# Kernel optimization log

Hardware: AMD Instinct MI355X
Metric: run time of the kernel (lower is better)

## Reference

```python
import jax, jax.numpy as jnp
import numpy as np

BLOCK = 64       # _aether_cfg['block_size']
JL_DIM = 32      # epsilon_jl_bridge d_out
EPS_GOV = 0.5    # fixed governor eps (governor.target)
ROPE_BASE = 10000.0
RMS_EPS = 1e-6


def _normalize(x, axis=-1):
    n = jnp.sqrt(jnp.sum(x * x, axis=axis, keepdims=True))
    return x / jnp.maximum(n, 1e-12)


def _rms_norm(x):
    return x * jax.lax.rsqrt(jnp.mean(x * x, axis=-1, keepdims=True) + RMS_EPS)


def _rope(x, cos, sin):
    half = x.shape[-1] // 2
    x1, x2 = x[..., :half], x[..., half:]
    return jnp.concatenate([x1 * cos + x2 * sin, -x1 * sin + x2 * cos], axis=-1)


def setup_inputs() -> dict:
    key = jax.random.key(0)
    ks = jax.random.split(key, 6)
    B, S, Dm, H = 2, 2048, 2048, 16
    sc = 1.0 / np.sqrt(Dm)
    x = jax.random.normal(ks[0], (B, S, Dm), jnp.float32)
    Wq = jax.random.normal(ks[1], (Dm, Dm), jnp.float32) * sc
    Wk = jax.random.normal(ks[2], (Dm, Dm), jnp.float32) * sc
    Wv = jax.random.normal(ks[3], (Dm, Dm), jnp.float32) * sc
    Wo = jax.random.normal(ks[4], (Dm, Dm), jnp.float32) * sc
    q_gain = jnp.ones((H,), jnp.float32)
    return {"x": x, "Wq": Wq, "Wk": Wk, "Wv": Wv, "Wo": Wo, "q_gain": q_gain}


def reference(x, Wq, Wk, Wv, Wo, q_gain):
    B, S, Dm = x.shape
    H = q_gain.shape[0]
    Dh = Dm // H

    # QKV projections (bias-free linear, torch weight layout [out,in])
    q = (x @ Wq.T).reshape(B, S, H, Dh).transpose(0, 2, 1, 3)  # (B,H,S,Dh)
    k = (x @ Wk.T).reshape(B, S, H, Dh).transpose(0, 2, 1, 3)
    v = (x @ Wv.T).reshape(B, S, H, Dh).transpose(0, 2, 1, 3)

    # RoPE tables
    inv_freq = 1.0 / (ROPE_BASE ** (jnp.arange(0, Dh, 2, dtype=jnp.float32) / Dh))
    freqs = jnp.outer(jnp.arange(S, dtype=jnp.float32), inv_freq)  # (S,Dh/2)
    cos = jnp.cos(freqs)[None, None]
    sin = jnp.sin(freqs)[None, None]

    q = _rope(_rms_norm(q), cos, sin) * q_gain[None, :, None, None]
    k = _rope(_rms_norm(k), cos, sin)

    # --- aether sparse SDPA: JL block bounds -> top-k blocks -> gather -> SDPA ---
    N = S // BLOCK  # number of KV blocks (static)
    proj = jax.random.normal(jax.random.key(42), (Dh, JL_DIM), jnp.float32) / np.sqrt(JL_DIM)

    q_proj = _normalize(q.mean(axis=2, keepdims=True) @ proj)          # (B,H,1,JL)
    k_blocks = k.reshape(B, H, N, BLOCK, Dh)
    k_proj = _normalize(k_blocks @ proj)                               # (B,H,N,BLOCK,JL)
    centroids = _normalize(k_proj.mean(axis=3))                        # (B,H,N,JL)
    radii = jnp.clip(
        1.0 - jnp.min(jnp.sum(k_proj * centroids[:, :, :, None, :], axis=-1), axis=-1),
        0.0, 1.0)                                                      # (B,H,N)
    ub = jnp.einsum('bhqj,bhnj->bhqn', q_proj, centroids) + radii[:, :, None, :]
    scores = ub[:, :, 0, :]                                            # (B,H,N)
    # force-include the last two blocks (union in the original code)
    scores = scores.at[:, :, N - 2:].set(jnp.inf)

    n_keep = max(2, int(N * min(1.0, EPS_GOV))) + 2                    # static
    _, top_idx = jax.lax.top_k(scores, n_keep)                         # (B,H,n_keep)
    top_idx = jnp.sort(top_idx, axis=-1)
    idx = (top_idx[..., None] * BLOCK + jnp.arange(BLOCK)).reshape(B, H, -1)  # (B,H,K)

    k_s = jnp.take_along_axis(k, idx[..., None], axis=2)               # (B,H,K,Dh)
    v_s = jnp.take_along_axis(v, idx[..., None], axis=2)

    att = jax.nn.softmax(
        jnp.einsum('bhqd,bhkd->bhqk', q, k_s) / np.sqrt(Dh), axis=-1)  # (B,H,S,K)
    y = jnp.einsum('bhqk,bhkd->bhqd', att, v_s)                        # (B,H,S,Dh)

    y = y.transpose(0, 2, 1, 3).reshape(B, S, Dm)
    return y @ Wo.T
```

## Files before the change

kernel.cpp:

```cpp
#include <hip/hip_runtime.h>
#include <hip/hip_bf16.h>

#define B_ 2
#define S_ 2048
#define DM 2048
#define H_ 16
#define DH 128
#define NBLK 32
#define NKEEP 18
#define BH (B_ * H_)

typedef __attribute__((ext_vector_type(8))) short short8;
typedef __attribute__((ext_vector_type(8))) _Float16 f16x8;
typedef __attribute__((ext_vector_type(4))) _Float16 f16x4;
typedef __attribute__((ext_vector_type(4))) float f32x4;

#define GLOAD16(gp, lp)                                                        \
  __builtin_amdgcn_global_load_lds(                                            \
      (const __attribute__((address_space(1))) unsigned int*)(const void*)(gp),\
      (__attribute__((address_space(3))) unsigned int*)(void*)(lp), 16, 0, 0)

__device__ __forceinline__ unsigned short f32_to_bf16(float f) {
  unsigned u = __float_as_uint(f);
  unsigned r = (u + 0x7fffu + ((u >> 16) & 1u)) >> 16;
  return (unsigned short)r;
}
__device__ __forceinline__ float bf16_to_f32(unsigned short h) {
  return __uint_as_float(((unsigned)h) << 16);
}

__device__ __forceinline__ unsigned rotl32(unsigned x, int r) {
  return (x << r) | (x >> (32 - r));
}

__device__ __forceinline__ float erfinv_f32(float x) {
  float w = -log1pf(-x * x);
  float p;
  if (w < 5.0f) {
    w -= 2.5f;
    p = 2.81022636e-08f;
    p = fmaf(p, w, 3.43273939e-07f);
    p = fmaf(p, w, -3.5233877e-06f);
    p = fmaf(p, w, -4.39150654e-06f);
    p = fmaf(p, w, 0.00021858087f);
    p = fmaf(p, w, -0.00125372503f);
    p = fmaf(p, w, -0.00417768164f);
    p = fmaf(p, w, 0.246640727f);
    p = fmaf(p, w, 1.50140941f);
  } else {
    w = sqrtf(w) - 3.0f;
    p = -0.000200214257f;
    p = fmaf(p, w, 0.000100950558f);
    p = fmaf(p, w, 0.00134934322f);
    p = fmaf(p, w, -0.00367342844f);
    p = fmaf(p, w, 0.00573950773f);
    p = fmaf(p, w, -0.0076224613f);
    p = fmaf(p, w, 0.00943887047f);
    p = fmaf(p, w, 1.00167406f);
    p = fmaf(p, w, 2.83297682f);
  }
  return p * x;
}

__device__ __forceinline__ float bits_to_normal(unsigned b) {
  float f = __uint_as_float((b >> 9) | 0x3f800000u) - 1.0f;
  const float lo = -0.9999999403953552f;
  float u = fmaxf(lo, fmaf(f, 2.0f, lo));
  return 1.4142135623730951f * erfinv_f32(u);
}

__global__ void proj_kernel(float* __restrict__ proj) {
  int i = blockIdx.x * blockDim.x + threadIdx.x;
  if (i >= 4096) return;
  unsigned k0 = 0u, k1 = 42u;
  unsigned k2 = 0x1BD11BDAu ^ k0 ^ k1;
  unsigned x0 = 0u, x1 = (unsigned)i;
  x0 += k0; x1 += k1;
#define QR(r) { x0 += x1; x1 = rotl32(x1, r); x1 ^= x0; }
  QR(13) QR(15) QR(26) QR(6)   x0 += k1; x1 += k2 + 1u;
  QR(17) QR(29) QR(16) QR(24)  x0 += k2; x1 += k0 + 2u;
  QR(13) QR(15) QR(26) QR(6)   x0 += k0; x1 += k1 + 3u;
  QR(17) QR(29) QR(16) QR(24)  x0 += k1; x1 += k2 + 4u;
  QR(13) QR(15) QR(26) QR(6)   x0 += k2; x1 += k0 + 5u;
#undef QR
  proj[i] = bits_to_normal(x0 ^ x1) / 5.656854249492381f;
}

__global__ void rope_table_kernel(float* __restrict__ cosb, float* __restrict__ sinb) {
  int s = blockIdx.x;
  int j = threadIdx.x;
  double e = (double)(2 * j) / 128.0;
  double invf = 1.0 / pow(10000.0, e);
  float freq = (float)s * (float)invf;
  cosb[s * 64 + j] = (float)cos((double)freq);
  sinb[s * 64 + j] = (float)sin((double)freq);
}

__global__ __launch_bounds__(256) void split_x3_kernel(const float* __restrict__ in,
                                                       unsigned short* __restrict__ hi,
                                                       unsigned short* __restrict__ lo,
                                                       _Float16* __restrict__ f16,
                                                       int n4) {
  int i = blockIdx.x * blockDim.x + threadIdx.x;
  if (i >= n4) return;
  float4 v = ((const float4*)in)[i];
  ushort4 hv, lv;
  f16x4 fv;
  hv.x = f32_to_bf16(v.x); lv.x = f32_to_bf16(v.x - bf16_to_f32(hv.x)); fv[0] = (_Float16)v.x;
  hv.y = f32_to_bf16(v.y); lv.y = f32_to_bf16(v.y - bf16_to_f32(hv.y)); fv[1] = (_Float16)v.y;
  hv.z = f32_to_bf16(v.z); lv.z = f32_to_bf16(v.z - bf16_to_f32(hv.z)); fv[2] = (_Float16)v.z;
  hv.w = f32_to_bf16(v.w); lv.w = f32_to_bf16(v.w - bf16_to_f32(hv.w)); fv[3] = (_Float16)v.w;
  ((ushort4*)hi)[i] = hv;
  ((ushort4*)lo)[i] = lv;
  ((f16x4*)f16)[i] = fv;
}

__global__ __launch_bounds__(256) void split_kernel(const float* __restrict__ in,
                                                    unsigned short* __restrict__ hi,
                                                    unsigned short* __restrict__ lo,
                                                    int n4) {
  int i = blockIdx.x * blockDim.x + threadIdx.x;
  if (i >= n4) return;
  float4 v = ((const float4*)in)[i];
  ushort4 hv, lv;
  hv.x = f32_to_bf16(v.x); lv.x = f32_to_bf16(v.x - bf16_to_f32(hv.x));
  hv.y = f32_to_bf16(v.y); lv.y = f32_to_bf16(v.y - bf16_to_f32(hv.y));
  hv.z = f32_to_bf16(v.z); lv.z = f32_to_bf16(v.z - bf16_to_f32(hv.z));
  hv.w = f32_to_bf16(v.w); lv.w = f32_to_bf16(v.w - bf16_to_f32(hv.w));
  ((ushort4*)hi)[i] = hv;
  ((ushort4*)lo)[i] = lv;
}

__global__ __launch_bounds__(256) void split_f16_kernel(const float* __restrict__ in,
                                                        _Float16* __restrict__ f16,
                                                        int n4) {
  int i = blockIdx.x * blockDim.x + threadIdx.x;
  if (i >= n4) return;
  float4 v = ((const float4*)in)[i];
  f16x4 fv;
  fv[0] = (_Float16)v.x; fv[1] = (_Float16)v.y;
  fv[2] = (_Float16)v.z; fv[3] = (_Float16)v.w;
  ((f16x4*)f16)[i] = fv;
}

__global__ __launch_bounds__(512, 2) void mfma_gemm_k_sk(const unsigned short* __restrict__ Ahi,
                                                         const unsigned short* __restrict__ Alo,
                                                         const unsigned short* __restrict__ Whi,
                                                         const unsigned short* __restrict__ Wlo,
                                                         float* __restrict__ kp0,
                                                         float* __restrict__ kp1) {
  __shared__ char smem[131072];
  const int t = threadIdx.x, l = t & 63, w = t >> 6;
  const int lin = blockIdx.z * 128 + blockIdx.y * 8 + blockIdx.x;
  const int swz = (lin & 7) * 32 + (lin >> 3);
  const int kz = swz >> 7;
  const int idx = swz & 127;
  const int n0 = (idx & 7) * 256;
  const int m0 = (idx >> 3) * 256;
  const int kbase = kz * 1024;
  float* C = kz ? kp1 : kp0;
  const int wm = w >> 2, wn = w & 3;
  const int lr = l & 15;
  const int lg8 = (l >> 4) * 8;
  const size_t rstep = (size_t)16 * DM;

  const unsigned short* gAh = Ahi + (size_t)(m0 + w * 32 + lr) * DM + lg8;
  const unsigned short* gAl = Alo + (size_t)(m0 + w * 32 + lr) * DM + lg8;
  const unsigned short* gBh = Whi + (size_t)(n0 + w * 32 + lr) * DM + lg8;
  const unsigned short* gBl = Wlo + (size_t)(n0 + w * 32 + lr) * DM + lg8;

  f32x4 acc[8][4];
#pragma unroll
  for (int i = 0; i < 8; ++i)
#pragma unroll
    for (int j = 0; j < 4; ++j) acc[i][j] = (f32x4){0.f, 0.f, 0.f, 0.f};

  {
    char* base = smem + w * 2048;
    GLOAD16(gAh + kbase, base);
    GLOAD16(gAh + rstep + kbase, base + 1024);
    GLOAD16(gAl + kbase, base + 16384);
    GLOAD16(gAl + rstep + kbase, base + 16384 + 1024);
    GLOAD16(gBh + kbase, base + 32768);
    GLOAD16(gBh + rstep + kbase, base + 32768 + 1024);
    GLOAD16(gBl + kbase, base + 49152);
    GLOAD16(gBl + rstep + kbase, base + 49152 + 1024);
  }
  int cur = 0;

#define KQUAD(q)                                                                        \
  {                                                                                     \
    short8 ah0 = *(const short8*)(buf + (wm * 8 + 2 * (q)) * 1024 + l * 16);            \
    short8 ah1 = *(const short8*)(buf + (wm * 8 + 2 * (q) + 1) * 1024 + l * 16);        \
    short8 al0 = *(const short8*)(buf + 16384 + (wm * 8 + 2 * (q)) * 1024 + l * 16);    \
    short8 al1 = *(const short8*)(buf + 16384 + (wm * 8 + 2 * (q) + 1) * 1024 + l * 16);\
    __builtin_amdgcn_s_setprio(1);                                                      \
    _Pragma("unroll")                                                                   \
    for (int n = 0; n < 4; ++n) {                                                       \
      acc[2 * (q)][n] = __builtin_amdgcn_mfma_f32_16x16x32_bf16(ah0, bh[n], acc[2 * (q)][n], 0, 0, 0); \
      acc[2 * (q)][n] = __builtin_amdgcn_mfma_f32_16x16x32_bf16(ah0, bl[n], acc[2 * (q)][n], 0, 0, 0); \
      acc[2 * (q)][n] = __builtin_amdgcn_mfma_f32_16x16x32_bf16(al0, bh[n], acc[2 * (q)][n], 0, 0, 0); \
    }                                                                                   \
    _Pragma("unroll")                                                                   \
    for (int n = 0; n < 4; ++n) {                                                       \
      acc[2 * (q) + 1][n] = __builtin_amdgcn_mfma_f32_16x16x32_bf16(ah1, bh[n], acc[2 * (q) + 1][n], 0, 0, 0); \
      acc[2 * (q) + 1][n] = __builtin_amdgcn_mfma_f32_16x16x32_bf16(ah1, bl[n], acc[2 * (q) + 1][n], 0, 0, 0); \
      acc[2 * (q) + 1][n] = __builtin_amdgcn_mfma_f32_16x16x32_bf16(al1, bh[n], acc[2 * (q) + 1][n], 0, 0, 0); \
    }                                                                                   \
    __builtin_amdgcn_s_setprio(0);                                                      \
  }

  for (int k0 = kbase; k0 < kbase + 1024; k0 += 32) {
    const bool more = (k0 + 32 < kbase + 1024);
    char* buf = smem + cur * 65536;
    char* nb = smem + (cur ^ 1) * 65536 + w * 2048;
    const int kn = k0 + 32;

    if (more) {
      GLOAD16(gBh + kn, nb + 32768);
      GLOAD16(gBh + rstep + kn, nb + 32768 + 1024);
      asm volatile("s_waitcnt vmcnt(2)" ::: "memory");
    } else {
      asm volatile("s_waitcnt vmcnt(0)" ::: "memory");
    }
    __builtin_amdgcn_s_barrier();

    short8 bh[4], bl[4];
#pragma unroll
    for (int f = 0; f < 4; ++f) {
      bh[f] = *(const short8*)(buf + 32768 + (wn * 4 + f) * 1024 + l * 16);
      bl[f] = *(const short8*)(buf + 49152 + (wn * 4 + f) * 1024 + l * 16);
    }
    KQUAD(0);
    __builtin_amdgcn_s_barrier();

    if (more) {
      GLOAD16(gBl + kn, nb + 49152);
      GLOAD16(gBl + rstep + kn, nb + 49152 + 1024);
    }
    KQUAD(1);
    __builtin_amdgcn_s_barrier();

    if (more) {
      GLOAD16(gAh + kn, nb);
      GLOAD16(gAh + rstep + kn, nb + 1024);
    }
    KQUAD(2);
    __builtin_amdgcn_s_barrier();

    if (more) {
      GLOAD16(gAl + kn, nb + 16384);
      GLOAD16(gAl + rstep + kn, nb + 16384 + 1024);
    }
    KQUAD(3);
    __builtin_amdgcn_s_barrier();

    cur ^= 1;
  }
#undef KQUAD

#pragma unroll
  for (int m = 0; m < 8; ++m) {
    int row0 = m0 + wm * 128 + m * 16 + (l >> 4) * 4;
#pragma unroll
    for (int n = 0; n < 4; ++n) {
      int col = n0 + wn * 64 + n * 16 + (l & 15);
      int h = col >> 7, d = col & 127;
#pragma unroll
      for (int r = 0; r < 4; ++r) {
        int mm = row0 + r;
        int b = mm >> 11, s = mm & (S_ - 1);
        C[(((size_t)(b * H_ + h) * S_) + s) * DH + d] = acc[m][n][r];
      }
    }
  }
}

__global__ __launch_bounds__(512, 2) void mfma_gemm_qv(const _Float16* __restrict__ A,
                                                       const _Float16* __restrict__ W,
                                                       float* __restrict__ Cq,
                                                       _Float16* __restrict__ vt) {
  __shared__ char smem[65536];
  const int t = threadIdx.x, l = t & 63, w = t >> 6;
  const int lin = blockIdx.y * gridDim.x + blockIdx.x;
  const int swz = (lin & 7) * 32 + (lin >> 3);
  const int n0 = (swz & 15) * 256;
  const int m0 = (swz >> 4) * 256;
  const int wm = w >> 2, wn = w & 3;
  const int lr = l & 15;
  const int lg8 = (l >> 4) * 8;
  const size_t rstep = (size_t)16 * DM;

  const _Float16* gA = A + (size_t)(m0 + w * 32 + lr) * DM + lg8;
  const _Float16* gB = W + (size_t)(n0 + w * 32 + lr) * DM + lg8;

  f32x4 acc[8][4];
#pragma unroll
  for (int i = 0; i < 8; ++i)
#pragma unroll
    for (int j = 0; j < 4; ++j) acc[i][j] = (f32x4){0.f, 0.f, 0.f, 0.f};

  {
    char* base = smem + w * 2048;
    GLOAD16(gA, base);
    GLOAD16(gA + rstep, base + 1024);
    GLOAD16(gB, base + 16384);
    GLOAD16(gB + rstep, base + 16384 + 1024);
  }
  int cur = 0;

  for (int k0 = 0; k0 < DM; k0 += 32) {
    const bool more = (k0 + 32 < DM);
    char* buf = smem + cur * 32768;
    char* nb = smem + (cur ^ 1) * 32768 + w * 2048;
    const int kn = k0 + 32;

    if (more) {
      GLOAD16(gA + kn, nb);
      GLOAD16(gA + rstep + kn, nb + 1024);
      asm volatile("s_waitcnt vmcnt(2)" ::: "memory");
    } else {
      asm volatile("s_waitcnt vmcnt(0)" ::: "memory");
    }
    __builtin_amdgcn_s_barrier();

    f16x8 b[4];
#pragma unroll
    for (int j = 0; j < 4; ++j)
      b[j] = *(const f16x8*)(buf + 16384 + (wn * 4 + j) * 1024 + l * 16);
    __builtin_amdgcn_s_setprio(1);
#pragma unroll
    for (int i = 0; i < 4; ++i) {
      f16x8 a = *(const f16x8*)(buf + (wm * 8 + i) * 1024 + l * 16);
#pragma unroll
      for (int j = 0; j < 4; ++j)
        acc[i][j] = __builtin_amdgcn_mfma_f32_16x16x32_f16(a, b[j], acc[i][j], 0, 0, 0);
    }
    __builtin_amdgcn_s_setprio(0);
    __builtin_amdgcn_s_barrier();

    if (more) {
      GLOAD16(gB + kn, nb + 16384);
      GLOAD16(gB + rstep + kn, nb + 16384 + 1024);
    }
    __builtin_amdgcn_s_setprio(1);
#pragma unroll
    for (int i = 4; i < 8; ++i) {
      f16x8 a = *(const f16x8*)(buf + (wm * 8 + i) * 1024 + l * 16);
#pragma unroll
      for (int j = 0; j < 4; ++j)
        acc[i][j] = __builtin_amdgcn_mfma_f32_16x16x32_f16(a, b[j], acc[i][j], 0, 0, 0);
    }
    __builtin_amdgcn_s_setprio(0);
    __builtin_amdgcn_s_barrier();

    cur ^= 1;
  }

#pragma unroll
  for (int m = 0; m < 8; ++m) {
    int row0 = m0 + wm * 128 + m * 16 + (l >> 4) * 4;
#pragma unroll
    for (int n = 0; n < 4; ++n) {
      int col = n0 + wn * 64 + n * 16 + (l & 15);
      if (col < DM) {
        int h = col >> 7, d = col & 127;
#pragma unroll
        for (int r = 0; r < 4; ++r) {
          int mm = row0 + r;
          int b2 = mm >> 11, s = mm & (S_ - 1);
          Cq[(((size_t)(b2 * H_ + h) * S_) + s) * DH + d] = acc[m][n][r];
        }
      } else {
        int vcol = col - DM;
        int h = vcol >> 7, d = vcol & 127;
        int b2 = row0 >> 11, s0 = row0 & (S_ - 1);
        f16x4 vv;
        vv[0] = (_Float16)acc[m][n][0];
        vv[1] = (_Float16)acc[m][n][1];
        vv[2] = (_Float16)acc[m][n][2];
        vv[3] = (_Float16)acc[m][n][3];
        *(f16x4*)(vt + (((size_t)(b2 * H_ + h)) * DH + d) * S_ + s0) = vv;
      }
    }
  }
}

template <int MODE>
__global__ __launch_bounds__(256) void mfma_gemm_f16(const _Float16* __restrict__ A,
                                                     const _Float16* __restrict__ W,
                                                     void* __restrict__ Cout) {
  __shared__ char smem[65536];
  const int t = threadIdx.x, l = t & 63, w = t >> 6;
  const int lin = blockIdx.y * gridDim.x + blockIdx.x;
  const int cpx = (gridDim.x * gridDim.y) >> 3;
  const int swz = (lin & 7) * cpx + (lin >> 3);
  const int n0 = (swz % gridDim.x) * 128;
  const int m0 = (swz / gridDim.x) * 128;
  const int wm = w >> 1, wn = w & 1;
  const int lr = l & 15;
  const int lg8 = (l >> 4) * 8;

  auto STAGE = [&](int k0, int c) {
    char* base = smem + c * 32768;
#pragma unroll
    for (int f0 = 0; f0 < 4; ++f0) {
      int f = w * 4 + f0;
      int rb = f >> 1, kh = f & 1;
      GLOAD16(A + (size_t)(m0 + rb * 16 + lr) * DM + k0 + kh * 32 + lg8,
              base + f * 1024);
      GLOAD16(W + (size_t)(n0 + rb * 16 + lr) * DM + k0 + kh * 32 + lg8,
              base + 16384 + f * 1024);
    }
  };

  f32x4 acc[4][4];
#pragma unroll
  for (int i = 0; i < 4; ++i)
#pragma unroll
    for (int j = 0; j < 4; ++j) acc[i][j] = (f32x4){0.f, 0.f, 0.f, 0.f};

  STAGE(0, 0);
  int cur = 0;

  for (int k0 = 0; k0 < DM; k0 += 64) {
    if (k0 + 64 < DM) {
      STAGE(k0 + 64, cur ^ 1);
      asm volatile("s_waitcnt vmcnt(8)" ::: "memory");
    } else {
      asm volatile("s_waitcnt vmcnt(0)" ::: "memory");
    }
    __builtin_amdgcn_s_barrier();

    char* buf = smem + cur * 32768;
    f16x8 a[4][2], b[4][2];
#pragma unroll
    for (int i = 0; i < 4; ++i)
#pragma unroll
      for (int kh = 0; kh < 2; ++kh) {
        a[i][kh] = *(const f16x8*)(buf + ((wm * 4 + i) * 2 + kh) * 1024 + l * 16);
        b[i][kh] = *(const f16x8*)(buf + 16384 + ((wn * 4 + i) * 2 + kh) * 1024 + l * 16);
      }
    __builtin_amdgcn_s_setprio(1);
#pragma unroll
    for (int i = 0; i < 4; ++i)
#pragma unroll
      for (int j = 0; j < 4; ++j) {
        acc[i][j] = __builtin_amdgcn_mfma_f32_16x16x32_f16(a[i][0], b[j][0], acc[i][j], 0, 0, 0);
        acc[i][j] = __builtin_amdgcn_mfma_f32_16x16x32_f16(a[i][1], b[j][1], acc[i][j], 0, 0, 0);
      }
    __builtin_amdgcn_s_setprio(0);
    __builtin_amdgcn_s_barrier();
    cur ^= 1;
  }

#pragma unroll
  for (int i = 0; i < 4; ++i) {
    int row0 = m0 + wm * 64 + i * 16 + (l >> 4) * 4;
#pragma unroll
    for (int j = 0; j < 4; ++j) {
      int col = n0 + wn * 64 + j * 16 + (l & 15);
      if constexpr (MODE == 1) {
        float* C = (float*)Cout;
#pragma unroll
        for (int r = 0; r < 4; ++r)
          C[(size_t)(row0 + r) * DM + col] = acc[i][j][r];
      }
    }
  }
}

__global__ __launch_bounds__(256) void rmsrope_k_kernel(float* __restrict__ k,
                                                        const float* __restrict__ kp1,
                                                        _Float16* __restrict__ kf,
                                                        const float* __restrict__ cosb,
                                                        const float* __restrict__ sinb) {
  int w = threadIdx.x >> 6;
  int lane = threadIdx.x & 63;
  long r = (long)blockIdx.x * 4 + w;
  float* p = k + r * DH;
  const float* p1 = kp1 + r * DH;
  int s = (int)(r & (S_ - 1));
  float x1 = p[lane] + p1[lane];
  float x2 = p[lane + 64] + p1[lane + 64];
  float ss = fmaf(x1, x1, x2 * x2);
#pragma unroll
  for (int off = 32; off; off >>= 1) ss += __shfl_xor(ss, off);
  float rms = rsqrtf(ss * (1.0f / 128.0f) + 1e-6f);
  float n1 = x1 * rms, n2 = x2 * rms;
  float c = cosb[s * 64 + lane], sn = sinb[s * 64 + lane];
  float o1 = fmaf(n1, c, n2 * sn);
  float o2 = fmaf(-n1, sn, n2 * c);
  p[lane] = o1;
  p[lane + 64] = o2;
  kf[r * DH + lane] = (_Float16)o1;
  kf[r * DH + lane + 64] = (_Float16)o2;
}

__global__ __launch_bounds__(256) void rmsrope_q_kernel(float* __restrict__ q,
                                                        const float* __restrict__ cosb,
                                                        const float* __restrict__ sinb,
                                                        const float* __restrict__ qg) {
  int w = threadIdx.x >> 6;
  int lane = threadIdx.x & 63;
  long r = (long)blockIdx.x * 4 + w;
  float* p = q + r * DH;
  int s = (int)(r & (S_ - 1));
  int h = (int)((r >> 11) & (H_ - 1));
  float x1 = p[lane], x2 = p[lane + 64];
  float ss = fmaf(x1, x1, x2 * x2);
#pragma unroll
  for (int off = 32; off; off >>= 1) ss += __shfl_xor(ss, off);
  float rms = rsqrtf(ss * (1.0f / 128.0f) + 1e-6f);
  float n1 = x1 * rms, n2 = x2 * rms;
  float c = cosb[s * 64 + lane], sn = sinb[s * 64 + lane];
  float g = qg[h];
  float o1 = fmaf(n1, c, n2 * sn) * g;
  float o2 = fmaf(-n1, sn, n2 * c) * g;
  p[lane] = o1;
  p[lane + 64] = o2;
}

__global__ __launch_bounds__(256) void qmean_part_kernel(const float* __restrict__ q,
                                                         float* __restrict__ partial) {
  __shared__ float red[256];
  const int bh = blockIdx.x >> 4, chunk = blockIdx.x & 15;
  const int t = threadIdx.x;
  const int d = t & 127, half = t >> 7;
  const float* qb = q + ((size_t)bh * S_ + chunk * 128 + half * 64) * DH;
  float sum = 0.0f;
#pragma unroll 4
  for (int s = 0; s < 64; ++s) sum += qb[(size_t)s * DH + d];
  red[t] = sum;
  __syncthreads();
  if (t < 128) partial[(size_t)blockIdx.x * 128 + t] = red[t] + red[t + 128];
}

__global__ void qproj_kernel(const float* __restrict__ partial,
                             const float* __restrict__ proj,
                             float* __restrict__ qp) {
  __shared__ float meanq[128];
  __shared__ float qps[32];
  __shared__ float nrm;
  const int bh = blockIdx.x, t = threadIdx.x;
  float s = 0.0f;
#pragma unroll
  for (int c = 0; c < 16; ++c) s += partial[((size_t)bh * 16 + c) * 128 + t];
  meanq[t] = s * (1.0f / 2048.0f);
  __syncthreads();
  if (t < 32) {
    float sum = 0.0f;
    for (int d = 0; d < 128; ++d) sum = fmaf(meanq[d], proj[d * 32 + t], sum);
    qps[t] = sum;
  }
  __syncthreads();
  if (t == 0) {
    float sum = 0.0f;
    for (int j = 0; j < 32; ++j) sum += qps[j] * qps[j];
    nrm = 1.0f / fmaxf(sqrtf(sum), 1e-12f);
  }
  __syncthreads();
  if (t < 32) qp[bh * 32 + t] = qps[t] * nrm;
}

__global__ __launch_bounds__(256) void kscore_kernel(const float* __restrict__ k,
                                                     const float* __restrict__ proj,
                                                     const float* __restrict__ qp,
                                                     float* __restrict__ scores) {
  __shared__ float ps[128][32];
  __shared__ float kp[64][33];
  __shared__ float cent[33];
  __shared__ float nrm;
  const int bh = blockIdx.x >> 5, n = blockIdx.x & 31;
  const int t = threadIdx.x;
  for (int i = t; i < 4096; i += 256) ps[i >> 5][i & 31] = proj[i];
  const float* kn = k + ((size_t)bh * S_ + n * 64) * DH;
  __syncthreads();
  {
    int row = t >> 2, j0 = (t & 3) * 8;
    float accv[8];
#pragma unroll
    for (int jj = 0; jj < 8; ++jj) accv[jj] = 0.0f;
#pragma unroll 4
    for (int d = 0; d < 128; ++d) {
      float kv = kn[(size_t)row * DH + d];
#pragma unroll
      for (int jj = 0; jj < 8; ++jj) accv[jj] = fmaf(kv, ps[d][j0 + jj], accv[jj]);
    }
#pragma unroll
    for (int jj = 0; jj < 8; ++jj) kp[row][j0 + jj] = accv[jj];
  }
  __syncthreads();
  if (t < 64) {
    float sum = 0.0f;
    for (int j = 0; j < 32; ++j) sum += kp[t][j] * kp[t][j];
    float scl = 1.0f / fmaxf(sqrtf(sum), 1e-12f);
    for (int j = 0; j < 32; ++j) kp[t][j] *= scl;
  }
  __syncthreads();
  if (t < 32) {
    float sum = 0.0f;
    for (int r2 = 0; r2 < 64; ++r2) sum += kp[r2][t];
    cent[t] = sum * (1.0f / 64.0f);
  }
  __syncthreads();
  if (t == 0) {
    float sum = 0.0f;
    for (int j = 0; j < 32; ++j) sum += cent[j] * cent[j];
    nrm = 1.0f / fmaxf(sqrtf(sum), 1e-12f);
  }
  __syncthreads();
  if (t < 32) cent[t] *= nrm;
  __syncthreads();
  if (t < 64) {
    float dt = 0.0f;
    for (int j = 0; j < 32; ++j) dt = fmaf(kp[t][j], cent[j], dt);
#pragma unroll
    for (int off = 32; off; off >>= 1) dt = fminf(dt, __shfl_xor(dt, off));
    if (t == 0) {
      float radius = fminf(fmaxf(1.0f - dt, 0.0f), 1.0f);
      float dq = 0.0f;
      for (int j = 0; j < 32; ++j) dq = fmaf(qp[bh * 32 + j], cent[j], dq);
      scores[bh * 32 + n] = dq + radius;
    }
  }
}

__global__ void topk_kernel(const float* __restrict__ scores, int* __restrict__ top_idx) {
  if (threadIdx.x != 0) return;
  const int bh = blockIdx.x;
  float sc[NBLK];
  for (int j = 0; j < NBLK; ++j) sc[j] = scores[bh * 32 + j];
  sc[NBLK - 2] = INFINITY;
  sc[NBLK - 1] = INFINITY;
  int chosen[NKEEP];
  bool used[NBLK];
  for (int j = 0; j < NBLK; ++j) used[j] = false;
  for (int kk = 0; kk < NKEEP; ++kk) {
    int best = -1;
    float bv = 0.0f;
    for (int j = 0; j < NBLK; ++j)
      if (!used[j] && (best < 0 || sc[j] > bv)) { bv = sc[j]; best = j; }
    used[best] = true;
    chosen[kk] = best;
  }
  for (int a = 1; a < NKEEP; ++a) {
    int v2 = chosen[a], b2 = a - 1;
    while (b2 >= 0 && chosen[b2] > v2) { chosen[b2 + 1] = chosen[b2]; --b2; }
    chosen[b2 + 1] = v2;
  }
  for (int a = 0; a < NKEEP; ++a) top_idx[bh * NKEEP + a] = chosen[a];
}

__global__ __launch_bounds__(256) void attn_mfma_kernel(const float* __restrict__ q,
                                                        const _Float16* __restrict__ kf,
                                                        const _Float16* __restrict__ vt,
                                                        const int* __restrict__ top_idx,
                                                        _Float16* __restrict__ yf) {
  __shared__ char lds[74752];
  const int bh = blockIdx.x >> 5;
  const int qt = blockIdx.x & 31;
  const int t = threadIdx.x, l = t & 63, w = t >> 6;
  const int lr = l & 15, lg = l >> 4;
  const float scale = 0.08838834764831843f;

  f16x8 qf[4];
  {
    const float* qbase = q + ((size_t)(bh * S_ + qt * 64 + w * 16 + lr)) * DH + lg * 8;
#pragma unroll
    for (int dc = 0; dc < 4; ++dc) {
      float4 v0 = *(const float4*)(qbase + dc * 32);
      float4 v1 = *(const float4*)(qbase + dc * 32 + 4);
      f16x8 h;
      h[0] = (_Float16)v0.x; h[1] = (_Float16)v0.y; h[2] = (_Float16)v0.z; h[3] = (_Float16)v0.w;
      h[4] = (_Float16)v1.x; h[5] = (_Float16)v1.y; h[6] = (_Float16)v1.z; h[7] = (_Float16)v1.w;
      qf[dc] = h;
    }
  }

  float m_[4] = {-INFINITY, -INFINITY, -INFINITY, -INFINITY};
  float ls[4] = {0.f, 0.f, 0.f, 0.f};
  f32x4 yacc[8];
#pragma unroll
  for (int dt = 0; dt < 8; ++dt) yacc[dt] = (f32x4){0.f, 0.f, 0.f, 0.f};

  char* Pw = lds + 65536 + w * 2304;

  const _Float16* kb0 = kf + (size_t)bh * S_ * DH;
  const _Float16* vb0 = vt + (size_t)bh * DH * S_;
  const int* idxp = top_idx + bh * NKEEP;

  auto STAGE = [&](int blk, int c) {
    char* base = lds + c * 32768;
#pragma unroll
    for (int f0 = 0; f0 < 4; ++f0) {
      int f = w * 4 + f0;
      int kt = f >> 2, dc = f & 3;
      GLOAD16(kb0 + (size_t)(blk * 64 + kt * 16 + lr) * DH + dc * 32 + lg * 8,
              base + f * 1024);
      int K0 = f >> 3, dt = f & 7;
      GLOAD16(vb0 + (size_t)(dt * 16 + lr) * S_ + blk * 64 + K0 * 32 + lg * 8,
              base + 16384 + f * 1024);
    }
  };

  int cur = 0;
  STAGE(idxp[0], 0);

  for (int it = 0; it < NKEEP; ++it) {
    if (it + 1 < NKEEP) {
      STAGE(idxp[it + 1], cur ^ 1);
      asm volatile("s_waitcnt vmcnt(8)" ::: "memory");
    } else {
      asm volatile("s_waitcnt vmcnt(0)" ::: "memory");
    }
    __builtin_amdgcn_s_barrier();
    char* buf = lds + cur * 32768;

    f32x4 sacc[4];
#pragma unroll
    for (int kt = 0; kt < 4; ++kt) sacc[kt] = (f32x4){0.f, 0.f, 0.f, 0.f};
    __builtin_amdgcn_s_setprio(1);
#pragma unroll
    for (int kt = 0; kt < 4; ++kt)
#pragma unroll
      for (int dc = 0; dc < 4; ++dc) {
        f16x8 kfr = *(const f16x8*)(buf + (kt * 4 + dc) * 1024 + l * 16);
        sacc[kt] = __builtin_amdgcn_mfma_f32_16x16x32_f16(qf[dc], kfr, sacc[kt], 0, 0, 0);
      }
    __builtin_amdgcn_s_setprio(0);

    float p[4][4];
#pragma unroll
    for (int r = 0; r < 4; ++r) {
      float mt = fmaxf(fmaxf(sacc[0][r], sacc[1][r]), fmaxf(sacc[2][r], sacc[3][r])) * scale;
#pragma unroll
      for (int off = 1; off < 16; off <<= 1) mt = fmaxf(mt, __shfl_xor(mt, off));
      float mn = fmaxf(m_[r], mt);
      float corr = __expf(m_[r] - mn);
      float rs = 0.f;
#pragma unroll
      for (int kt = 0; kt < 4; ++kt) {
        p[kt][r] = __expf(fmaf(sacc[kt][r], scale, -mn));
        rs += p[kt][r];
      }
#pragma unroll
      for (int off = 1; off < 16; off <<= 1) rs += __shfl_xor(rs, off);
      ls[r] = ls[r] * corr + rs;
      m_[r] = mn;
#pragma unroll
      for (int dt = 0; dt < 8; ++dt) yacc[dt][r] *= corr;
    }

#pragma unroll
    for (int kt = 0; kt < 4; ++kt)
#pragma unroll
      for (int r = 0; r < 4; ++r)
        *(_Float16*)(Pw + (lg * 4 + r) * 144 + (kt * 16 + lr) * 2) = (_Float16)p[kt][r];

    __builtin_amdgcn_s_setprio(1);
#pragma unroll
    for (int K0 = 0; K0 < 2; ++K0) {
      f16x8 pa = *(const f16x8*)(Pw + lr * 144 + K0 * 64 + lg * 16);
#pragma unroll
      for (int dt = 0; dt < 8; ++dt) {
        f16x8 vf = *(const f16x8*)(buf + 16384 + (K0 * 8 + dt) * 1024 + l * 16);
        yacc[dt] = __builtin_amdgcn_mfma_f32_16x16x32_f16(pa, vf, yacc[dt], 0, 0, 0);
      }
    }
    __builtin_amdgcn_s_setprio(0);

    __builtin_amdgcn_s_barrier();
    cur ^= 1;
  }

  const int b = bh >> 4, h = bh & (H_ - 1);
  float inv[4];
#pragma unroll
  for (int r = 0; r < 4; ++r) inv[r] = 1.0f / ls[r];
#pragma unroll
  for (int r = 0; r < 4; ++r) {
    int srow = qt * 64 + w * 16 + lg * 4 + r;
    size_t off0 = ((size_t)b * S_ + srow) * DM + h * DH + lr;
#pragma unroll
    for (int dt = 0; dt < 8; ++dt)
      yf[off0 + dt * 16] = (_Float16)(yacc[dt][r] * inv[r]);
  }
}

extern "C" void kernel_launch(void* const* d_in, const int* in_sizes, int n_in,
                              void* d_out, int out_size, void* d_ws, size_t ws_size,
                              hipStream_t stream) {
  const float* x  = (const float*)d_in[0];
  const float* Wq = (const float*)d_in[1];
  const float* Wk = (const float*)d_in[2];
  const float* Wv = (const float*)d_in[3];
  const float* Wo = (const float*)d_in[4];
  const float* qg = (const float*)d_in[5];
  float* out = (float*)d_out;

  const size_t NE = (size_t)BH * S_ * DH;
  const size_t WE = (size_t)DM * DM;
  char* p = (char*)d_ws;
  float* q_ws = (float*)p; p += NE * 4;
  float* k_ws = (float*)p; p += NE * 4;
  unsigned short* xhi = (unsigned short*)p; p += NE * 2;
  unsigned short* xlo = (unsigned short*)p; p += NE * 2;
  _Float16* xf16 = (_Float16*)p; p += NE * 2;
  unsigned short* wkhi = (unsigned short*)p; p += WE * 2;
  unsigned short* wklo = (unsigned short*)p; p += WE * 2;
  _Float16* wqv = (_Float16*)p; p += 2 * WE * 2;
  float* cosb = (float*)p; p += (size_t)S_ * 64 * 4;
  float* sinb = (float*)p; p += (size_t)S_ * 64 * 4;
  float* projb = (float*)p; p += 4096 * 4;
  int* idxb = (int*)p; p += BH * NKEEP * 4;
  float* scores = (float*)p; p += BH * NBLK * 4;
  float* qpbuf = (float*)p; p += BH * 32 * 4;
  float* qpart = cosb;
  float* kpart1 = q_ws;
  _Float16* kf16 = (_Float16*)wkhi;
  _Float16* vt = (_Float16*)xlo;
  _Float16* yf16 = (_Float16*)xhi;
  _Float16* wo = wqv;

  const int nx4 = (int)(NE / 4);
  const int nw4 = (int)(WE / 4);

  proj_kernel<<<dim3(16), dim3(256), 0, stream>>>(projb);
  rope_table_kernel<<<dim3(S_), dim3(64), 0, stream>>>(cosb, sinb);
  split_x3_kernel<<<dim3(nx4 / 256), dim3(256), 0, stream>>>(x, xhi, xlo, xf16, nx4);
  split_kernel<<<dim3(nw4 / 256), dim3(256), 0, stream>>>(Wk, wkhi, wklo, nw4);
  split_f16_kernel<<<dim3(nw4 / 256), dim3(256), 0, stream>>>(Wq, wqv, nw4);
  split_f16_kernel<<<dim3(nw4 / 256), dim3(256), 0, stream>>>(Wv, wqv + WE, nw4);

  mfma_gemm_k_sk<<<dim3(8, 16, 2), dim3(512), 0, stream>>>(xhi, xlo, wkhi, wklo,
                                                           k_ws, kpart1);

  rmsrope_k_kernel<<<dim3((BH * S_) / 4), dim3(256), 0, stream>>>(k_ws, kpart1, kf16, cosb, sinb);

  mfma_gemm_qv<<<dim3(16, 16), dim3(512), 0, stream>>>(xf16, wqv, q_ws, vt);

  rmsrope_q_kernel<<<dim3((BH * S_) / 4), dim3(256), 0, stream>>>(q_ws, cosb, sinb, qg);

  qmean_part_kernel<<<dim3(BH * 16), dim3(256), 0, stream>>>(q_ws, qpart);
  qproj_kernel<<<dim3(BH), dim3(128), 0, stream>>>(qpart, projb, qpbuf);
  kscore_kernel<<<dim3(BH * NBLK), dim3(256), 0, stream>>>(k_ws, projb, qpbuf, scores);
  topk_kernel<<<dim3(BH), dim3(64), 0, stream>>>(scores, idxb);

  attn_mfma_kernel<<<dim3(BH * 32), dim3(256), 0, stream>>>(q_ws, kf16, vt, idxb, yf16);

  split_f16_kernel<<<dim3(nw4 / 256), dim3(256), 0, stream>>>(Wo, wo, nw4);
  mfma_gemm_f16<1><<<dim3(16, 32), dim3(256), 0, stream>>>(yf16, wo, out);
}
```

Baseline: 448.5 us.

## Double attention query tile per block and skip softmax rescale when max is stable

The attention kernel now runs 512 threads (8 waves) per block over 128 query rows, so each staged K/V tile in LDS is shared by twice as many queries and each thread issues half as many global-to-LDS loads. The online softmax also gains a lazy-rescale path: when every row's new max stays within 8 of the running max across the whole wave, the correction exponentials and accumulator rescaling are skipped. The grid is halved to 512 blocks, which lowers parallelism, and the lazy path lets intermediate values grow by up to about e^8 in fp16 P and fp32 accumulators.

Result: no change. 454.1 us (+1.2%).

```diff
diff --git a/kernel.cpp b/kernel.cpp
--- a/kernel.cpp
+++ b/kernel.cpp
@@ -652,21 +652,21 @@
   for (int a = 0; a < NKEEP; ++a) top_idx[bh * NKEEP + a] = chosen[a];
 }
 
-__global__ __launch_bounds__(256) void attn_mfma_kernel(const float* __restrict__ q,
-                                                        const _Float16* __restrict__ kf,
-                                                        const _Float16* __restrict__ vt,
-                                                        const int* __restrict__ top_idx,
-                                                        _Float16* __restrict__ yf) {
-  __shared__ char lds[74752];
-  const int bh = blockIdx.x >> 5;
-  const int qt = blockIdx.x & 31;
+__global__ __launch_bounds__(512, 1) void attn_mfma_kernel(const float* __restrict__ q,
+                                                           const _Float16* __restrict__ kf,
+                                                           const _Float16* __restrict__ vt,
+                                                           const int* __restrict__ top_idx,
+                                                           _Float16* __restrict__ yf) {
+  __shared__ char lds[83968];
+  const int bh = blockIdx.x >> 4;
+  const int qt = blockIdx.x & 15;
   const int t = threadIdx.x, l = t & 63, w = t >> 6;
   const int lr = l & 15, lg = l >> 4;
   const float scale = 0.08838834764831843f;
 
   f16x8 qf[4];
   {
-    const float* qbase = q + ((size_t)(bh * S_ + qt * 64 + w * 16 + lr)) * DH + lg * 8;
+    const float* qbase = q + ((size_t)(bh * S_ + qt * 128 + w * 16 + lr)) * DH + lg * 8;
 #pragma unroll
     for (int dc = 0; dc < 4; ++dc) {
       float4 v0 = *(const float4*)(qbase + dc * 32);
@@ -693,8 +693,8 @@
   auto STAGE = [&](int blk, int c) {
     char* base = lds + c * 32768;
 #pragma unroll
-    for (int f0 = 0; f0 < 4; ++f0) {
-      int f = w * 4 + f0;
+    for (int f0 = 0; f0 < 2; ++f0) {
+      int f = w * 2 + f0;
       int kt = f >> 2, dc = f & 3;
       GLOAD16(kb0 + (size_t)(blk * 64 + kt * 16 + lr) * DH + dc * 32 + lg * 8,
               base + f * 1024);
@@ -710,7 +710,7 @@
   for (int it = 0; it < NKEEP; ++it) {
     if (it + 1 < NKEEP) {
       STAGE(idxp[it + 1], cur ^ 1);
-      asm volatile("s_waitcnt vmcnt(8)" ::: "memory");
+      asm volatile("s_waitcnt vmcnt(4)" ::: "memory");
     } else {
       asm volatile("s_waitcnt vmcnt(0)" ::: "memory");
     }
@@ -730,26 +730,48 @@
       }
     __builtin_amdgcn_s_setprio(0);
 
+    float mt[4];
+#pragma unroll
+    for (int r = 0; r < 4; ++r) {
+      float mv = fmaxf(fmaxf(sacc[0][r], sacc[1][r]), fmaxf(sacc[2][r], sacc[3][r])) * scale;
+#pragma unroll
+      for (int off = 1; off < 16; off <<= 1) mv = fmaxf(mv, __shfl_xor(mv, off));
+      mt[r] = mv;
+    }
     float p[4][4];
-#pragma unroll
-    for (int r = 0; r < 4; ++r) {
-      float mt = fmaxf(fmaxf(sacc[0][r], sacc[1][r]), fmaxf(sacc[2][r], sacc[3][r])) * scale;
-#pragma unroll
-      for (int off = 1; off < 16; off <<= 1) mt = fmaxf(mt, __shfl_xor(mt, off));
-      float mn = fmaxf(m_[r], mt);
-      float corr = __expf(m_[r] - mn);
-      float rs = 0.f;
-#pragma unroll
-      for (int kt = 0; kt < 4; ++kt) {
-        p[kt][r] = __expf(fmaf(sacc[kt][r], scale, -mn));
-        rs += p[kt][r];
+    bool ok = (mt[0] <= m_[0] + 8.0f) && (mt[1] <= m_[1] + 8.0f) &&
+              (mt[2] <= m_[2] + 8.0f) && (mt[3] <= m_[3] + 8.0f);
+    if (__all(ok)) {
+#pragma unroll
+      for (int r = 0; r < 4; ++r) {
+        float rs = 0.f;
+#pragma unroll
+        for (int kt = 0; kt < 4; ++kt) {
+          p[kt][r] = __expf(fmaf(sacc[kt][r], scale, -m_[r]));
+          rs += p[kt][r];
+        }
+#pragma unroll
+        for (int off = 1; off < 16; off <<= 1) rs += __shfl_xor(rs, off);
+        ls[r] += rs;
       }
-#pragma unroll
-      for (int off = 1; off < 16; off <<= 1) rs += __shfl_xor(rs, off);
-      ls[r] = ls[r] * corr + rs;
-      m_[r] = mn;
-#pragma unroll
-      for (int dt = 0; dt < 8; ++dt) yacc[dt][r] *= corr;
+    } else {
+#pragma unroll
+      for (int r = 0; r < 4; ++r) {
+        float mn = fmaxf(m_[r], mt[r]);
+        float corr = __expf(m_[r] - mn);
+        float rs = 0.f;
+#pragma unroll
+        for (int kt = 0; kt < 4; ++kt) {
+          p[kt][r] = __expf(fmaf(sacc[kt][r], scale, -mn));
+          rs += p[kt][r];
+        }
+#pragma unroll
+        for (int off = 1; off < 16; off <<= 1) rs += __shfl_xor(rs, off);
+        ls[r] = ls[r] * corr + rs;
+        m_[r] = mn;
+#pragma unroll
+        for (int dt = 0; dt < 8; ++dt) yacc[dt][r] *= corr;
+      }
     }
 
 #pragma unroll
@@ -780,7 +802,7 @@
   for (int r = 0; r < 4; ++r) inv[r] = 1.0f / ls[r];
 #pragma unroll
   for (int r = 0; r < 4; ++r) {
-    int srow = qt * 64 + w * 16 + lg * 4 + r;
+    int srow = qt * 128 + w * 16 + lg * 4 + r;
     size_t off0 = ((size_t)b * S_ + srow) * DM + h * DH + lr;
 #pragma unroll
     for (int dt = 0; dt < 8; ++dt)
@@ -847,7 +869,7 @@
   kscore_kernel<<<dim3(BH * NBLK), dim3(256), 0, stream>>>(k_ws, projb, qpbuf, scores);
   topk_kernel<<<dim3(BH), dim3(64), 0, stream>>>(scores, idxb);
 
-  attn_mfma_kernel<<<dim3(BH * 32), dim3(256), 0, stream>>>(q_ws, kf16, vt, idxb, yf16);
+  attn_mfma_kernel<<<dim3(BH * 16), dim3(512), 0, stream>>>(q_ws, kf16, vt, idxb, yf16);
 
   split_f16_kernel<<<dim3(nw4 / 256), dim3(256), 0, stream>>>(Wo, wo, nw4);
   mfma_gemm_f16<1><<<dim3(16, 32), dim3(256), 0, stream>>>(yf16, wo, out);
```
